# Performance work log

Measured on AMD Instinct MI355X. Metric: run time of the kernel, lower is better.

The kernel has to match this reference:

```python
import jax, jax.numpy as jnp
import numpy as np

B, M, T, H = 32, 2048, 8, 64  # batch, measurements, num_tags, hidden_dim
LATENT, TRIL = 3, 6
NEG_INF = -1e9  # masked-out logit value for segment softmax


def _linear_init(key, fan_in, fan_out):
    # torch nn.Linear default: U(-1/sqrt(fan_in), 1/sqrt(fan_in)) for W and b
    bound = 1.0 / np.sqrt(fan_in)
    kw, kb = jax.random.split(key)
    w = jax.random.uniform(kw, (fan_in, fan_out), minval=-bound, maxval=bound, dtype=jnp.float32)
    b = jax.random.uniform(kb, (fan_out,), minval=-bound, maxval=bound, dtype=jnp.float32)
    return w, b


def setup_inputs() -> dict:
    key = jax.random.key(0)
    ks = jax.random.split(key, 14)
    inp = {}
    inp['measurements'] = jax.random.normal(ks[0], (B, M, 5), dtype=jnp.float32)
    inp['measurement_to_tag_mapping'] = jax.random.randint(ks[1], (B, M), 0, T, dtype=jnp.int32)
    inp['me_w1'], inp['me_b1'] = _linear_init(ks[2], 5, H)
    inp['me_w2'], inp['me_b2'] = _linear_init(ks[3], H, H)
    inp['q_w'], inp['q_b'] = _linear_init(ks[4], H, H)
    inp['k_w'], inp['k_b'] = _linear_init(ks[5], H, H)
    inp['v_w'], inp['v_b'] = _linear_init(ks[6], H, H)
    inp['a1_w1'], inp['a1_b1'] = _linear_init(ks[7], H, H // 2)
    inp['a1_w2'], inp['a1_b2'] = _linear_init(ks[8], H // 2, 1)
    inp['a2_w1'], inp['a2_b1'] = _linear_init(ks[9], H, H // 2)
    inp['a2_w2'], inp['a2_b2'] = _linear_init(ks[10], H // 2, 1)
    inp['mu_w'], inp['mu_b'] = _linear_init(ks[11], H, LATENT)
    inp['logL_w'], inp['logL_b'] = _linear_init(ks[12], H, TRIL)
    return inp


def reference(measurements, measurement_to_tag_mapping,
              me_w1, me_b1, me_w2, me_b2,
              q_w, q_b, k_w, k_b, v_w, v_b,
              a1_w1, a1_b1, a1_w2, a1_b2,
              a2_w1, a2_b1, a2_w2, a2_b2,
              mu_w, mu_b, logL_w, logL_b):
    # measurement encoder: two Linear+ReLU layers -> [B, M, H]
    feat = jax.nn.relu(measurements @ me_w1 + me_b1)
    feat = jax.nn.relu(feat @ me_w2 + me_b2)

    # self-attention with residual
    q = feat @ q_w + q_b
    k = feat @ k_w + k_b
    v = feat @ v_w + v_b
    scale = jnp.sqrt(jnp.float32(H))
    scores = jnp.einsum('bmh,bnh->bmn', q, k) / scale  # [B, M, M]
    feat = feat + jnp.einsum('bmn,bnh->bmh', jax.nn.softmax(scores, axis=-1), v)

    # per-measurement attention logits (attention_net1) -> [B, M]
    a1 = (jax.nn.relu(feat @ a1_w1 + a1_b1) @ a1_w2 + a1_b2)[..., 0]

    # segment softmax per tag id: mask [B, M, T]
    tag_mask = measurement_to_tag_mapping[..., None] == jnp.arange(T)
    seg_logits = jnp.where(tag_mask, a1[..., None], NEG_INF)
    seg_w = jax.nn.softmax(seg_logits, axis=1)  # softmax over measurements within each tag
    tag_feat = jnp.einsum('bmt,bmh->bth', seg_w, feat)  # [B, T, H]

    # aggregate tags (attention_net2) -> pose feature [B, H]
    a2 = (jax.nn.relu(tag_feat @ a2_w1 + a2_b1) @ a2_w2 + a2_b2)[..., 0]  # [B, T]
    tag_w = jax.nn.softmax(a2, axis=-1)
    pose = jnp.einsum('bt,bth->bh', tag_w, tag_feat)

    mu = pose @ mu_w + mu_b
    logL = pose @ logL_w + logL_b
    return mu, logL
```

## Files before the change

kernel.cpp:

```cpp
#include <hip/hip_runtime.h>
#include <hip/hip_bf16.h>
#include <cstdint>
#include <cstddef>


typedef short s16x8 __attribute__((ext_vector_type(8)));
typedef float f32x4 __attribute__((ext_vector_type(4)));
typedef float f32x16 __attribute__((ext_vector_type(16)));

#define LOG2E  1.4426950408889634f
#define QSCALE 0.18033688011112042f

__device__ __forceinline__ unsigned short f2bf(float f) {
    unsigned u = __builtin_bit_cast(unsigned, f);
    u += 0x7fffu + ((u >> 16) & 1u);
    return (unsigned short)(u >> 16);
}

__device__ __forceinline__ unsigned cvtpk(float lo, float hi) {
    unsigned r;
    asm("v_cvt_pk_bf16_f32 %0, %1, %2" : "=v"(r) : "v"(lo), "v"(hi));
    return r;
}

__device__ __forceinline__ float exp2_raw(float x) {
    float r;
    asm("v_exp_f32 %0, %1" : "=v"(r) : "v"(x));
    return r;
}

#define PLSWAP(a, b) asm("v_permlane32_swap_b32 %0, %1" : "+v"(a), "+v"(b))

__device__ __forceinline__ void gload_lds16(const void* g, void* l) {
    __builtin_amdgcn_global_load_lds((const __attribute__((address_space(1))) void*)g,
                                     (__attribute__((address_space(3))) void*)l, 16, 0, 0);
}

#define MFMA16(a, b, c) __builtin_amdgcn_mfma_f32_16x16x32_bf16((a), (b), (c), 0, 0, 0)
#define MFMA32(a, b, c) __builtin_amdgcn_mfma_f32_32x32x16_bf16((a), (b), (c), 0, 0, 0)

__global__ void k_prep(const float* __restrict__ w2, const float* __restrict__ qw,
                       const float* __restrict__ kw, const float* __restrict__ vw,
                       const float* __restrict__ a1w1,
                       unsigned short* __restrict__ wt, float* __restrict__ a1w1t)
{
    int tid = threadIdx.x;
    for (int idx = tid; idx < 4096; idx += 256) {
        int o = idx >> 6, i = idx & 63;
        wt[idx]         = f2bf(w2[i * 64 + o]);
        wt[4096 + idx]  = f2bf(qw[i * 64 + o] * QSCALE);
        wt[8192 + idx]  = f2bf(kw[i * 64 + o]);
        wt[12288 + idx] = f2bf(vw[i * 64 + o]);
    }
    for (int idx = tid; idx < 2048; idx += 256) {
        int j = idx >> 6, d = idx & 63;
        a1w1t[idx] = a1w1[d * 32 + j];
    }
}

__global__ __launch_bounds__(256)
void k_encode(const float* __restrict__ meas, const float* __restrict__ w1,
              const float* __restrict__ b1, const float* __restrict__ b2,
              const float* __restrict__ qb, const float* __restrict__ kb,
              const float* __restrict__ vb,
              const unsigned short* __restrict__ wt,
              float* __restrict__ feat,
              unsigned short* __restrict__ qbf, unsigned short* __restrict__ kbf,
              unsigned short* __restrict__ vt)
{
    __shared__ __align__(16) unsigned short hbuf[4][1152];
    int tid = threadIdx.x;
    int w = tid >> 6, lane = tid & 63;
    int g = lane >> 4, c16 = lane & 15;
    int m0 = (blockIdx.x * 4 + w) * 16;
    int b  = m0 >> 11;
    unsigned short* hb = hbuf[w];

    float x[5];
    const float* xr = meas + (size_t)(m0 + c16) * 5;
#pragma unroll
    for (int i = 0; i < 5; ++i) x[i] = xr[i];
    s16x8 aH[2];
#pragma unroll
    for (int s = 0; s < 2; ++s) {
#pragma unroll
        for (int jj = 0; jj < 8; ++jj) {
            int j = 8 * g + jj + 32 * s;
            float acc = b1[j];
#pragma unroll
            for (int i = 0; i < 5; ++i) acc += x[i] * w1[i * 64 + j];
            aH[s][jj] = (short)f2bf(fmaxf(acc, 0.f));
        }
    }

    const f32x4 zero = {0.f, 0.f, 0.f, 0.f};
    f32x4 c[4];

#pragma unroll
    for (int dt = 0; dt < 4; ++dt) {
        c[dt] = zero;
#pragma unroll
        for (int s = 0; s < 2; ++s) {
            s16x8 bf = *(const s16x8*)(wt + (c16 + 16 * dt) * 64 + 32 * s + 8 * g);
            c[dt] = MFMA16(aH[s], bf, c[dt]);
        }
    }
#pragma unroll
    for (int dt = 0; dt < 4; ++dt) {
        int d = c16 + 16 * dt;
        float bias = b2[d];
#pragma unroll
        for (int r = 0; r < 4; ++r) {
            float v = fmaxf(c[dt][r] + bias, 0.f);
            feat[(size_t)(m0 + 4 * g + r) * 64 + d] = v;
            hb[(4 * g + r) * 72 + d] = f2bf(v);
        }
    }
    s16x8 aF[2];
#pragma unroll
    for (int s = 0; s < 2; ++s)
        aF[s] = *(const s16x8*)(hb + c16 * 72 + 32 * s + 8 * g);

    auto gemmW = [&](const unsigned short* wmat, f32x4* cc) {
#pragma unroll
        for (int dt = 0; dt < 4; ++dt) {
            cc[dt] = zero;
#pragma unroll
            for (int s = 0; s < 2; ++s) {
                s16x8 bf = *(const s16x8*)(wmat + (c16 + 16 * dt) * 64 + 32 * s + 8 * g);
                cc[dt] = MFMA16(aF[s], bf, cc[dt]);
            }
        }
    };

    gemmW(wt + 4096, c);
#pragma unroll
    for (int dt = 0; dt < 4; ++dt) {
        int d = c16 + 16 * dt;
        float bias = qb[d] * QSCALE;
#pragma unroll
        for (int r = 0; r < 4; ++r)
            qbf[(size_t)(m0 + 4 * g + r) * 64 + d] = f2bf(c[dt][r] + bias);
    }
    gemmW(wt + 8192, c);
#pragma unroll
    for (int dt = 0; dt < 4; ++dt) {
        int d = c16 + 16 * dt;
        float bias = kb[d];
#pragma unroll
        for (int r = 0; r < 4; ++r)
            kbf[(size_t)(m0 + 4 * g + r) * 64 + d] = f2bf(c[dt][r] + bias);
    }
    gemmW(wt + 12288, c);
#pragma unroll
    for (int dt = 0; dt < 4; ++dt) {
        int d = c16 + 16 * dt;
        float bias = vb[d];
#pragma unroll
        for (int r = 0; r < 4; ++r)
            hb[(4 * g + r) * 72 + d] = f2bf(c[dt][r] + bias);
    }
    unsigned short tvv[16];
#pragma unroll
    for (int mr = 0; mr < 16; ++mr) tvv[mr] = hb[mr * 72 + lane];
    s16x8 v0, v1;
#pragma unroll
    for (int e2 = 0; e2 < 8; ++e2) { v0[e2] = (short)tvv[e2]; v1[e2] = (short)tvv[8 + e2]; }
    unsigned short* dst = vt + ((size_t)b * 64 + lane) * 2048 + (m0 & 2047);
    *(s16x8*)dst = v0;
    *(s16x8*)(dst + 8) = v1;
}

__global__ __launch_bounds__(512, 4)
void k_attn(const unsigned short* __restrict__ qbf, const unsigned short* __restrict__ kbf,
            const unsigned short* __restrict__ vt, float* __restrict__ feat)
{
    __shared__ __align__(16) char smem[37888];

    int tid = threadIdx.x;
    int w_ = tid >> 6, lane = tid & 63;
    int h = lane >> 5, c32 = lane & 31;
    int jhalf = w_ & 1, tile = w_ >> 1;
    int b = blockIdx.x >> 4;
    int q0g = (blockIdx.x & 15) * 128 + tile * 32;
    size_t rowbase = (size_t)b * 2048;

    const unsigned short* kbf_b = kbf + rowbase * 64;
    const unsigned short* vt_b  = vt + (size_t)b * 64 * 2048;

    s16x8 qf[4];
    {
        const unsigned short* qp = qbf + (rowbase + q0g + c32) * 64 + 8 * h;
#pragma unroll
        for (int st = 0; st < 4; ++st)
            qf[st] = *(const s16x8*)(qp + 16 * st);
    }

    f32x16 zero16;
#pragma unroll
    for (int i = 0; i < 16; ++i) zero16[i] = 0.f;

    f32x16 o[2];
#pragma unroll
    for (int dt = 0; dt < 2; ++dt)
#pragma unroll
        for (int i = 0; i < 16; ++i) o[dt][i] = 0.f;
    float ll = 0.f;

    int srow = 8 * w_ + (lane >> 3);
    int scol = (lane & 7) ^ (srow & 7);
    const unsigned short* gk0 = kbf_b + (size_t)srow * 64 + scol * 8;
    const unsigned short* gv0 = vt_b + (size_t)srow * 2048 + scol * 8;

    auto stage = [&](int kt, int buf) {
        gload_lds16(gk0 + (size_t)kt * 4096, smem + buf * 8192 + w_ * 1024);
        gload_lds16(gv0 + kt * 64, smem + 16384 + buf * 8192 + w_ * 1024);
    };

    stage(0, 0);
    __syncthreads();

    int swz = c32 & 7;
    int krow = 32 * jhalf + c32;

    for (int kt = 0; kt < 32; ++kt) {
        int cur = kt & 1;
        if (kt + 1 < 32) stage(kt + 1, cur ^ 1);

        const char* Kb = smem + cur * 8192;
        const char* Vb = smem + 16384 + cur * 8192;

        s16x8 kf[4], vf[2][2];
#pragma unroll
        for (int st = 0; st < 4; ++st)
            kf[st] = *(const s16x8*)(Kb + krow * 128 + (((2 * st + h) ^ swz) * 16));
#pragma unroll
        for (int ks = 0; ks < 2; ++ks)
#pragma unroll
            for (int dt = 0; dt < 2; ++dt)
                vf[ks][dt] = *(const s16x8*)(Vb + (32 * dt + c32) * 128 +
                                             (((4 * jhalf + 2 * ks + h) ^ swz) * 16));

        __builtin_amdgcn_s_setprio(1);
        f32x16 sc = MFMA32(kf[0], qf[0], zero16);
#pragma unroll
        for (int st = 1; st < 4; ++st)
            sc = MFMA32(kf[st], qf[st], sc);
        __builtin_amdgcn_s_setprio(0);

        float p[16];
#pragma unroll
        for (int i = 0; i < 16; ++i) p[i] = exp2_raw(sc[i]);

        float s;
        {
            float a0 = p[0] + p[1],  a1 = p[2] + p[3],  a2 = p[4] + p[5],  a3 = p[6] + p[7];
            float a4 = p[8] + p[9],  a5 = p[10] + p[11], a6 = p[12] + p[13], a7 = p[14] + p[15];
            float b0 = a0 + a1, b1 = a2 + a3, b2 = a4 + a5, b3 = a6 + a7;
            s = (b0 + b1) + (b2 + b3);
        }
        {
            float s1 = s, s2 = s;
            PLSWAP(s1, s2);
            s = s1 + s2;
        }
        ll += s;

        unsigned u[8];
#pragma unroll
        for (int k2 = 0; k2 < 8; ++k2) u[k2] = cvtpk(p[2 * k2], p[2 * k2 + 1]);

        __builtin_amdgcn_s_setprio(1);
#pragma unroll
        for (int ks = 0; ks < 2; ++ks) {
            unsigned a0 = u[4 * ks + 0], b0 = u[4 * ks + 2];
            unsigned a1 = u[4 * ks + 1], b1 = u[4 * ks + 3];
            PLSWAP(a0, b0);
            PLSWAP(a1, b1);
            union { unsigned uu[4]; s16x8 v; } pa;
            pa.uu[0] = a0; pa.uu[1] = a1; pa.uu[2] = b0; pa.uu[3] = b1;
#pragma unroll
            for (int dt = 0; dt < 2; ++dt)
                o[dt] = MFMA32(pa.v, vf[ks][dt], o[dt]);
        }
        __builtin_amdgcn_s_setprio(0);
        __syncthreads();
    }

    float* Om = (float*)smem;
    float* Ml = (float*)(smem + 36864);
    if (jhalf) {
#pragma unroll
        for (int dt = 0; dt < 2; ++dt)
#pragma unroll
            for (int rg = 0; rg < 4; ++rg) {
                f32x4 vv;
#pragma unroll
                for (int r = 0; r < 4; ++r) vv[r] = o[dt][4 * rg + r];
                *(f32x4*)&Om[(tile * 64 + 32 * dt + c32) * 36 + 8 * rg + 4 * h] = vv;
            }
        if (h == 0) Ml[tile * 32 + c32] = ll;
    }
    __syncthreads();
    if (!jhalf) {
        float l1 = Ml[tile * 32 + c32];
        float f = 1.f / (ll + l1);
        float fr[16];
#pragma unroll
        for (int r = 0; r < 16; ++r) {
            int qrow = (r & 3) + 8 * (r >> 2) + 4 * h;
            fr[r] = __shfl(f, qrow);
        }
#pragma unroll
        for (int dt = 0; dt < 2; ++dt)
#pragma unroll
            for (int rg = 0; rg < 4; ++rg) {
                f32x4 pv = *(const f32x4*)&Om[(tile * 64 + 32 * dt + c32) * 36 + 8 * rg + 4 * h];
#pragma unroll
                for (int r = 0; r < 4; ++r) {
                    int rr = 4 * rg + r;
                    int qrow = r + 8 * rg + 4 * h;
                    size_t fi = (rowbase + q0g + qrow) * 64 + 32 * dt + c32;
                    feat[fi] += (o[dt][rr] + pv[r]) * fr[rr];
                }
            }
    }
}

__global__ __launch_bounds__(256)
void k_a1(const float* __restrict__ feat, const float* __restrict__ w1t,
          const float* __restrict__ b1, const float* __restrict__ w2,
          const float* __restrict__ b2, float* __restrict__ a1)
{
    int m = blockIdx.x * 256 + threadIdx.x;
    const f32x4* fr = (const f32x4*)(feat + (size_t)m * 64);

    float acc[32];
#pragma unroll
    for (int j = 0; j < 32; ++j) acc[j] = b1[j];

#pragma unroll
    for (int kc = 0; kc < 16; ++kc) {
        f32x4 f = fr[kc];
#pragma unroll
        for (int ki = 0; ki < 4; ++ki) {
            float fk = f[ki];
            int k = kc * 4 + ki;
#pragma unroll
            for (int j = 0; j < 32; ++j)
                acc[j] = fmaf(fk, w1t[j * 64 + k], acc[j]);
        }
    }
    float s = b2[0];
#pragma unroll
    for (int j = 0; j < 32; ++j) s += fmaxf(acc[j], 0.f) * w2[j];
    a1[m] = s;
}

__global__ __launch_bounds__(256)
void k_seg(const float* __restrict__ a1, const int* __restrict__ map,
           float* __restrict__ segstats)
{
    __shared__ float wred[4][8];
    __shared__ float MXs[8];
    int b = blockIdx.x;
    int tid = threadIdx.x, lane = tid & 63, w = tid >> 6;
    const float* a1b = a1 + b * 2048;
    const int* mp = map + b * 2048;

    float mx[8];
#pragma unroll
    for (int t = 0; t < 8; ++t) mx[t] = -1e9f;
    for (int m = tid; m < 2048; m += 256) {
        float v = a1b[m];
        int tg = mp[m];
#pragma unroll
        for (int t = 0; t < 8; ++t)
            if (tg == t) mx[t] = fmaxf(mx[t], v);
    }
#pragma unroll
    for (int t = 0; t < 8; ++t) {
        float v = mx[t];
        v = fmaxf(v, __shfl_xor(v, 1));  v = fmaxf(v, __shfl_xor(v, 2));
        v = fmaxf(v, __shfl_xor(v, 4));  v = fmaxf(v, __shfl_xor(v, 8));
        v = fmaxf(v, __shfl_xor(v, 16)); v = fmaxf(v, __shfl_xor(v, 32));
        mx[t] = v;
    }
    if (lane == 0) {
#pragma unroll
        for (int t = 0; t < 8; ++t) wred[w][t] = mx[t];
    }
    __syncthreads();
    if (tid < 8) {
        float v = fmaxf(fmaxf(wred[0][tid], wred[1][tid]),
                        fmaxf(wred[2][tid], wred[3][tid]));
        MXs[tid] = v;
        segstats[b * 16 + tid] = v;
    }
    __syncthreads();

    float sm[8];
#pragma unroll
    for (int t = 0; t < 8; ++t) sm[t] = 0.f;
    for (int m = tid; m < 2048; m += 256) {
        float v = a1b[m];
        int tg = mp[m];
        float e = exp2f((v - MXs[tg]) * LOG2E);
#pragma unroll
        for (int t = 0; t < 8; ++t)
            if (tg == t) sm[t] += e;
    }
#pragma unroll
    for (int t = 0; t < 8; ++t) {
        float v = sm[t];
        v += __shfl_xor(v, 1);  v += __shfl_xor(v, 2);
        v += __shfl_xor(v, 4);  v += __shfl_xor(v, 8);
        v += __shfl_xor(v, 16); v += __shfl_xor(v, 32);
        sm[t] = v;
    }
    __syncthreads();
    if (lane == 0) {
#pragma unroll
        for (int t = 0; t < 8; ++t) wred[w][t] = sm[t];
    }
    __syncthreads();
    if (tid < 8)
        segstats[b * 16 + 8 + tid] =
            1.f / (wred[0][tid] + wred[1][tid] + wred[2][tid] + wred[3][tid]);
}

__global__ __launch_bounds__(256)
void k_tagfeat(const float* __restrict__ a1, const int* __restrict__ map,
               const float* __restrict__ feat, const float* __restrict__ segstats,
               float* __restrict__ part)
{
    __shared__ float accv[4][8][64];
    __shared__ float MXs[8], SMIs[8];
    int b = blockIdx.x >> 4;
    int c = blockIdx.x & 15;
    int tid = threadIdx.x, lane = tid & 63, w = tid >> 6;

    if (tid < 16) {
        float v = segstats[b * 16 + tid];
        if (tid < 8) MXs[tid] = v; else SMIs[tid - 8] = v;
    }
    __syncthreads();

    const float* a1b = a1 + b * 2048;
    const int* mp = map + b * 2048;
    int m0 = c * 128;

    float tacc[8];
#pragma unroll
    for (int t = 0; t < 8; ++t) tacc[t] = 0.f;
    for (int mi = w; mi < 128; mi += 4) {
        int m = m0 + mi;
        float v = a1b[m];
        int tg = mp[m];
        float wgt = exp2f((v - MXs[tg]) * LOG2E) * SMIs[tg];
        float wf = wgt * feat[((size_t)b * 2048 + m) * 64 + lane];
#pragma unroll
        for (int t = 0; t < 8; ++t)
            if (tg == t) tacc[t] += wf;
    }
#pragma unroll
    for (int t = 0; t < 8; ++t) accv[w][t][lane] = tacc[t];
    __syncthreads();
    for (int e = tid; e < 512; e += 256) {
        int t = e >> 6, d = e & 63;
        part[((size_t)c * 32 + b) * 512 + e] =
            accv[0][t][d] + accv[1][t][d] + accv[2][t][d] + accv[3][t][d];
    }
}

__global__ __launch_bounds__(256)
void k_head(const float* __restrict__ part,
            const float* __restrict__ a2w1, const float* __restrict__ a2b1,
            const float* __restrict__ a2w2, const float* __restrict__ a2b2,
            const float* __restrict__ muw, const float* __restrict__ mub,
            const float* __restrict__ lLw, const float* __restrict__ lLb,
            float* __restrict__ out)
{
    __shared__ float tf[8][64];
    __shared__ float sc8[8];
    __shared__ float pose[64];
    int b = blockIdx.x;
    int tid = threadIdx.x;

    for (int e = tid; e < 512; e += 256) {
        float s = 0.f;
#pragma unroll
        for (int c = 0; c < 16; ++c) s += part[((size_t)c * 32 + b) * 512 + e];
        tf[e >> 6][e & 63] = s;
    }
    __syncthreads();

    {
        int t = tid >> 5, j = tid & 31;
        float acc = a2b1[j];
        for (int d = 0; d < 64; ++d) acc += tf[t][d] * a2w1[d * 32 + j];
        float hsum = fmaxf(acc, 0.f) * a2w2[j];
        hsum += __shfl_xor(hsum, 1);
        hsum += __shfl_xor(hsum, 2);
        hsum += __shfl_xor(hsum, 4);
        hsum += __shfl_xor(hsum, 8);
        hsum += __shfl_xor(hsum, 16);
        if (j == 0) sc8[t] = hsum + a2b2[0];
    }
    __syncthreads();
    if (tid < 64) {
        float smax = sc8[0];
#pragma unroll
        for (int t = 1; t < 8; ++t) smax = fmaxf(smax, sc8[t]);
        float e[8], ssum = 0.f;
#pragma unroll
        for (int t = 0; t < 8; ++t) { e[t] = exp2f((sc8[t] - smax) * LOG2E); ssum += e[t]; }
        float rinv = 1.f / ssum;
        float p = 0.f;
#pragma unroll
        for (int t = 0; t < 8; ++t) p += (e[t] * rinv) * tf[t][tid];
        pose[tid] = p;
    }
    __syncthreads();
    if (tid < 3) {
        float acc = mub[tid];
        for (int d = 0; d < 64; ++d) acc += pose[d] * muw[d * 3 + tid];
        out[b * 3 + tid] = acc;
    }
    if (tid >= 32 && tid < 38) {
        int oo = tid - 32;
        float acc = lLb[oo];
        for (int d = 0; d < 64; ++d) acc += pose[d] * lLw[d * 6 + oo];
        out[96 + b * 6 + oo] = acc;
    }
}

extern "C" void kernel_launch(void* const* d_in, const int* in_sizes, int n_in,
                              void* d_out, int out_size, void* d_ws, size_t ws_size,
                              hipStream_t stream)
{
    (void)in_sizes; (void)n_in; (void)out_size; (void)ws_size;

    const float* measurements = (const float*)d_in[0];
    const int*   mapping      = (const int*)d_in[1];
    const float* me_w1 = (const float*)d_in[2];
    const float* me_b1 = (const float*)d_in[3];
    const float* me_w2 = (const float*)d_in[4];
    const float* me_b2 = (const float*)d_in[5];
    const float* q_w   = (const float*)d_in[6];
    const float* q_b   = (const float*)d_in[7];
    const float* k_w   = (const float*)d_in[8];
    const float* k_b   = (const float*)d_in[9];
    const float* v_w   = (const float*)d_in[10];
    const float* v_b   = (const float*)d_in[11];
    const float* a1_w1 = (const float*)d_in[12];
    const float* a1_b1 = (const float*)d_in[13];
    const float* a1_w2 = (const float*)d_in[14];
    const float* a1_b2 = (const float*)d_in[15];
    const float* a2_w1 = (const float*)d_in[16];
    const float* a2_b1 = (const float*)d_in[17];
    const float* a2_w2 = (const float*)d_in[18];
    const float* a2_b2 = (const float*)d_in[19];
    const float* mu_w  = (const float*)d_in[20];
    const float* mu_b  = (const float*)d_in[21];
    const float* logL_w = (const float*)d_in[22];
    const float* logL_b = (const float*)d_in[23];

    char* ws = (char*)d_ws;
    unsigned short* wt    = (unsigned short*)(ws);
    float*          a1w1t = (float*)(ws + 32768);
    float*          feat  = (float*)(ws + 40960);
    unsigned short* qbf   = (unsigned short*)(ws + 16818176);
    unsigned short* kbf   = (unsigned short*)(ws + 25206784);
    unsigned short* vt    = (unsigned short*)(ws + 33595392);
    float*          a1    = (float*)(ws + 41984000);
    float*          segst = (float*)(ws + 42246144);
    float*          part  = (float*)(ws + 42248192);
    float*          out   = (float*)d_out;

    k_prep<<<1, 256, 0, stream>>>(me_w2, q_w, k_w, v_w, a1_w1, wt, a1w1t);
    k_encode<<<1024, 256, 0, stream>>>(measurements, me_w1, me_b1, me_b2, q_b, k_b, v_b,
                                       wt, feat, qbf, kbf, vt);
    k_attn<<<512, 512, 0, stream>>>(qbf, kbf, vt, feat);
    k_a1<<<256, 256, 0, stream>>>(feat, a1w1t, a1_b1, a1_w2, a1_b2, a1);
    k_seg<<<32, 256, 0, stream>>>(a1, mapping, segst);
    k_tagfeat<<<512, 256, 0, stream>>>(a1, mapping, feat, segst, part);
    k_head<<<32, 256, 0, stream>>>(part, a2_w1, a2_b1, a2_w2, a2_b2,
                                   mu_w, mu_b, logL_w, logL_b, out);
}
```

Baseline: 126.1 us.

## Halve attention block size and compute softmax row sums with an MFMA

The attention kernel moves from 512-thread blocks covering 128 queries to 256-thread blocks covering 64 queries, doubling the grid so each wave stages two K/V rows per tile. The row-sum of exponentials, previously a scalar add tree plus a lane swap, is now an extra MFMA against a bf16 ones vector. The main loop is also unrolled by two. This is meant to improve occupancy and load balance and to take VALU work off the critical path, at the cost of extra matrix-core work, more K/V reloads per query, and row sums taken from bf16-rounded probabilities.

Result: slower. 139.0 us (+10.2%).

```diff
diff --git a/kernel.cpp b/kernel.cpp
--- a/kernel.cpp
+++ b/kernel.cpp
@@ -171,18 +171,18 @@
     *(s16x8*)(dst + 8) = v1;
 }
 
-__global__ __launch_bounds__(512, 4)
+__global__ __launch_bounds__(256, 4)
 void k_attn(const unsigned short* __restrict__ qbf, const unsigned short* __restrict__ kbf,
             const unsigned short* __restrict__ vt, float* __restrict__ feat)
 {
-    __shared__ __align__(16) char smem[37888];
+    __shared__ __align__(16) char smem[32768];
 
     int tid = threadIdx.x;
     int w_ = tid >> 6, lane = tid & 63;
     int h = lane >> 5, c32 = lane & 31;
     int jhalf = w_ & 1, tile = w_ >> 1;
-    int b = blockIdx.x >> 4;
-    int q0g = (blockIdx.x & 15) * 128 + tile * 32;
+    int b = blockIdx.x >> 5;
+    int q0g = (blockIdx.x & 31) * 64 + tile * 32;
     size_t rowbase = (size_t)b * 2048;
 
     const unsigned short* kbf_b = kbf + rowbase * 64;
@@ -200,21 +200,33 @@
 #pragma unroll
     for (int i = 0; i < 16; ++i) zero16[i] = 0.f;
 
-    f32x16 o[2];
+    s16x8 onesB;
+#pragma unroll
+    for (int i = 0; i < 8; ++i) onesB[i] = (short)0x3F80;
+
+    f32x16 o[2], ol;
 #pragma unroll
     for (int dt = 0; dt < 2; ++dt)
 #pragma unroll
         for (int i = 0; i < 16; ++i) o[dt][i] = 0.f;
-    float ll = 0.f;
-
-    int srow = 8 * w_ + (lane >> 3);
-    int scol = (lane & 7) ^ (srow & 7);
-    const unsigned short* gk0 = kbf_b + (size_t)srow * 64 + scol * 8;
-    const unsigned short* gv0 = vt_b + (size_t)srow * 2048 + scol * 8;
+#pragma unroll
+    for (int i = 0; i < 16; ++i) ol[i] = 0.f;
+
+    int sr = lane >> 3;
+    int srowA = 16 * w_ + sr;
+    int scol  = (lane & 7) ^ (sr & 7);
+    const unsigned short* gkA = kbf_b + (size_t)srowA * 64 + scol * 8;
+    const unsigned short* gkB = gkA + 8 * 64;
+    const unsigned short* gvA = vt_b + (size_t)srowA * 2048 + scol * 8;
+    const unsigned short* gvB = gvA + 8 * 2048;
 
     auto stage = [&](int kt, int buf) {
-        gload_lds16(gk0 + (size_t)kt * 4096, smem + buf * 8192 + w_ * 1024);
-        gload_lds16(gv0 + kt * 64, smem + 16384 + buf * 8192 + w_ * 1024);
+        char* kd = smem + buf * 8192 + (2 * w_) * 1024;
+        char* vd = smem + 16384 + buf * 8192 + (2 * w_) * 1024;
+        gload_lds16(gkA + (size_t)kt * 4096, kd);
+        gload_lds16(gkB + (size_t)kt * 4096, kd + 1024);
+        gload_lds16(gvA + kt * 64, vd);
+        gload_lds16(gvB + kt * 64, vd + 1024);
     };
 
     stage(0, 0);
@@ -223,6 +235,7 @@
     int swz = c32 & 7;
     int krow = 32 * jhalf + c32;
 
+#pragma unroll 2
     for (int kt = 0; kt < 32; ++kt) {
         int cur = kt & 1;
         if (kt + 1 < 32) stage(kt + 1, cur ^ 1);
@@ -251,20 +264,6 @@
         float p[16];
 #pragma unroll
         for (int i = 0; i < 16; ++i) p[i] = exp2_raw(sc[i]);
-
-        float s;
-        {
-            float a0 = p[0] + p[1],  a1 = p[2] + p[3],  a2 = p[4] + p[5],  a3 = p[6] + p[7];
-            float a4 = p[8] + p[9],  a5 = p[10] + p[11], a6 = p[12] + p[13], a7 = p[14] + p[15];
-            float b0 = a0 + a1, b1 = a2 + a3, b2 = a4 + a5, b3 = a6 + a7;
-            s = (b0 + b1) + (b2 + b3);
-        }
-        {
-            float s1 = s, s2 = s;
-            PLSWAP(s1, s2);
-            s = s1 + s2;
-        }
-        ll += s;
 
         unsigned u[8];
 #pragma unroll
@@ -279,6 +278,7 @@
             PLSWAP(a1, b1);
             union { unsigned uu[4]; s16x8 v; } pa;
             pa.uu[0] = a0; pa.uu[1] = a1; pa.uu[2] = b0; pa.uu[3] = b1;
+            ol = MFMA32(pa.v, onesB, ol);
 #pragma unroll
             for (int dt = 0; dt < 2; ++dt)
                 o[dt] = MFMA32(pa.v, vf[ks][dt], o[dt]);
@@ -288,7 +288,7 @@
     }
 
     float* Om = (float*)smem;
-    float* Ml = (float*)(smem + 36864);
+    float* Ml = (float*)(smem + 18432);
     if (jhalf) {
 #pragma unroll
         for (int dt = 0; dt < 2; ++dt)
@@ -299,17 +299,21 @@
                 for (int r = 0; r < 4; ++r) vv[r] = o[dt][4 * rg + r];
                 *(f32x4*)&Om[(tile * 64 + 32 * dt + c32) * 36 + 8 * rg + 4 * h] = vv;
             }
-        if (h == 0) Ml[tile * 32 + c32] = ll;
+        if (c32 == 0) {
+#pragma unroll
+            for (int r = 0; r < 16; ++r) {
+                int qrow = (r & 3) + 8 * (r >> 2) + 4 * h;
+                Ml[tile * 32 + qrow] = ol[r];
+            }
+        }
     }
     __syncthreads();
     if (!jhalf) {
-        float l1 = Ml[tile * 32 + c32];
-        float f = 1.f / (ll + l1);
         float fr[16];
 #pragma unroll
         for (int r = 0; r < 16; ++r) {
             int qrow = (r & 3) + 8 * (r >> 2) + 4 * h;
-            fr[r] = __shfl(f, qrow);
+            fr[r] = 1.f / (ol[r] + Ml[tile * 32 + qrow]);
         }
 #pragma unroll
         for (int dt = 0; dt < 2; ++dt)
@@ -581,7 +585,7 @@
     k_prep<<<1, 256, 0, stream>>>(me_w2, q_w, k_w, v_w, a1_w1, wt, a1w1t);
     k_encode<<<1024, 256, 0, stream>>>(measurements, me_w1, me_b1, me_b2, q_b, k_b, v_b,
                                        wt, feat, qbf, kbf, vt);
-    k_attn<<<512, 512, 0, stream>>>(qbf, kbf, vt, feat);
+    k_attn<<<1024, 256, 0, stream>>>(qbf, kbf, vt, feat);
     k_a1<<<256, 256, 0, stream>>>(feat, a1w1t, a1_b1, a1_w2, a1_b2, a1);
     k_seg<<<32, 256, 0, stream>>>(a1, mapping, segst);
     k_tagfeat<<<512, 256, 0, stream>>>(a1, mapping, feat, segst, part);
```
